# Performance work log

Measured on AMD Instinct MI355X. Metric: run time of the kernel, lower is better.

Reference implementation:

```python
import jax, jax.numpy as jnp
import numpy as np

B, T, D, H, F = 4, 2048, 512, 8, 2048
WINDOW = 128
HD = D // H
EPS = 1e-5


def layer_norm(x, g, b):
    mu = jnp.mean(x, axis=-1, keepdims=True)
    var = jnp.mean(jnp.square(x - mu), axis=-1, keepdims=True)
    return (x - mu) * jax.lax.rsqrt(var + EPS) * g + b


def setup_inputs() -> dict:
    key = jax.random.key(0)
    ks = jax.random.split(key, 5)
    s = 0.02
    return {
        "x": jax.random.normal(ks[0], (B, T, D), dtype=jnp.float32),
        "in_proj_w": jax.random.normal(ks[1], (3 * D, D), dtype=jnp.float32) * s,
        "in_proj_b": jnp.zeros((3 * D,), dtype=jnp.float32),
        "out_w": jax.random.normal(ks[2], (D, D), dtype=jnp.float32) * s,
        "out_b": jnp.zeros((D,), dtype=jnp.float32),
        "ln1_g": jnp.ones((D,), dtype=jnp.float32),
        "ln1_b": jnp.zeros((D,), dtype=jnp.float32),
        "ln2_g": jnp.ones((D,), dtype=jnp.float32),
        "ln2_b": jnp.zeros((D,), dtype=jnp.float32),
        "w1": jax.random.normal(ks[3], (F, D), dtype=jnp.float32) * s,
        "b1": jnp.zeros((F,), dtype=jnp.float32),
        "w2": jax.random.normal(ks[4], (D, F), dtype=jnp.float32) * s,
        "b2": jnp.zeros((D,), dtype=jnp.float32),
    }


def reference(x, in_proj_w, in_proj_b, out_w, out_b, ln1_g, ln1_b, ln2_g, ln2_b, w1, b1, w2, b2):
    # pre-norm sliding-window causal self-attention
    x2 = layer_norm(x, ln1_g, ln1_b)
    qkv = x2 @ in_proj_w.T + in_proj_b  # (B,T,3D)
    q, k, v = jnp.split(qkv, 3, axis=-1)
    q = q.reshape(B, T, H, HD)
    k = k.reshape(B, T, H, HD)
    v = v.reshape(B, T, H, HD)
    scale = 1.0 / np.sqrt(HD).astype(np.float32)
    scores = jnp.einsum("bthd,bshd->bhts", q, k) * scale  # dense (B,H,T,T)
    idx = jnp.arange(T)
    i = idx[:, None]
    j = idx[None, :]
    allowed = (j <= i) & (j >= i - WINDOW + 1)  # (T,T) bool, True = attend
    scores = jnp.where(allowed[None, None], scores, -jnp.inf)
    attn = jax.nn.softmax(scores, axis=-1)
    ctx = jnp.einsum("bhts,bshd->bthd", attn, v).reshape(B, T, D)
    attn_out = ctx @ out_w.T + out_b
    x = x + attn_out  # dropout is identity in eval
    # FFN block
    x3 = layer_norm(x, ln2_g, ln2_b)
    h = jax.nn.gelu(x3 @ w1.T + b1, approximate=False)
    x = x + h @ w2.T + b2
    return x
```

## Files before the change

kernel.cpp:

```cpp
#include <hip/hip_runtime.h>
#include <math.h>

constexpr int Bn = 4;
constexpr int Tn = 2048;
constexpr int Dn = 512;
constexpr int Hn = 8;
constexpr int HDn = 64;
constexpr int Fn = 2048;
constexpr int WIN = 128;
constexpr float EPS = 1e-5f;
constexpr int Mrows = Bn * Tn;
constexpr int QKVD = 3 * Dn;

using short8 = __attribute__((ext_vector_type(8))) short;
using f32x4  = __attribute__((ext_vector_type(4))) float;

__device__ __forceinline__ short f2bf(float f) {
    unsigned u = __float_as_uint(f);
    unsigned r = (u + 0x7FFFu + ((u >> 16) & 1u)) >> 16;
    return (short)r;
}

__device__ __forceinline__ float gelu_fast(float v) {
    float u = 1.5957691216f * v * (1.0f + 0.044715f * v * v);
    float t = 1.0f - 2.0f / (__expf(u) + 1.0f);
    return 0.5f * v * (1.0f + t);
}

__device__ __forceinline__ void async16(const short* g, short* l) {
    __builtin_amdgcn_global_load_lds(
        (const __attribute__((address_space(1))) void*)g,
        (__attribute__((address_space(3))) void*)l,
        16, 0, 0);
}

__global__ __launch_bounds__(256) void cvt_all(const float* __restrict__ s0,
                                               const float* __restrict__ s1,
                                               const float* __restrict__ s2,
                                               const float* __restrict__ s3,
                                               short* __restrict__ d0,
                                               short* __restrict__ d1,
                                               short* __restrict__ d2,
                                               short* __restrict__ d3)
{
    int i = blockIdx.x * 256 + threadIdx.x;
    const float* src; short* dst; int j;
    if (i < 196608)      { src = s0; dst = d0; j = i; }
    else if (i < 262144) { src = s1; dst = d1; j = i - 196608; }
    else if (i < 524288) { src = s2; dst = d2; j = i - 262144; }
    else                 { src = s3; dst = d3; j = i - 524288; }
    float4 v = ((const float4*)src)[j];
    short4 o;
    o.x = f2bf(v.x); o.y = f2bf(v.y); o.z = f2bf(v.z); o.w = f2bf(v.w);
    ((short4*)dst)[j] = o;
}

__global__ __launch_bounds__(64) void ln_kernel(const float* __restrict__ x,
                                                const float* __restrict__ g,
                                                const float* __restrict__ b,
                                                short* __restrict__ y)
{
    int row = blockIdx.x;
    int lane = threadIdx.x;
    const float4* xr = (const float4*)(x + (size_t)row * Dn);
    float4 v0 = xr[lane];
    float4 v1 = xr[lane + 64];
    float s = v0.x + v0.y + v0.z + v0.w + v1.x + v1.y + v1.z + v1.w;
#pragma unroll
    for (int off = 32; off >= 1; off >>= 1) s += __shfl_xor(s, off, 64);
    float mu = s * (1.0f / Dn);
    float d0x = v0.x - mu, d0y = v0.y - mu, d0z = v0.z - mu, d0w = v0.w - mu;
    float d1x = v1.x - mu, d1y = v1.y - mu, d1z = v1.z - mu, d1w = v1.w - mu;
    float q = d0x*d0x + d0y*d0y + d0z*d0z + d0w*d0w
            + d1x*d1x + d1y*d1y + d1z*d1z + d1w*d1w;
#pragma unroll
    for (int off = 32; off >= 1; off >>= 1) q += __shfl_xor(q, off, 64);
    float inv = rsqrtf(q * (1.0f / Dn) + EPS);
    const float4* gr = (const float4*)g;
    const float4* br = (const float4*)b;
    float4 g0 = gr[lane], g1 = gr[lane + 64];
    float4 b0 = br[lane], b1 = br[lane + 64];
    short4 a0, a1;
    a0.x = f2bf(d0x * inv * g0.x + b0.x);
    a0.y = f2bf(d0y * inv * g0.y + b0.y);
    a0.z = f2bf(d0z * inv * g0.z + b0.z);
    a0.w = f2bf(d0w * inv * g0.w + b0.w);
    a1.x = f2bf(d1x * inv * g1.x + b1.x);
    a1.y = f2bf(d1y * inv * g1.y + b1.y);
    a1.z = f2bf(d1z * inv * g1.z + b1.z);
    a1.w = f2bf(d1w * inv * g1.w + b1.w);
    short4* yr = (short4*)(y + (size_t)row * Dn);
    yr[lane] = a0;
    yr[lane + 64] = a1;
}

__global__ __launch_bounds__(256) void gemm_res(const short* __restrict__ A,
                                                const short* __restrict__ Bw,
                                                const float* __restrict__ bias,
                                                const float* __restrict__ resid,
                                                float* __restrict__ Cf,
                                                int M, int N, int K)
{
    constexpr int BK = 64;
    constexpr int NCH = 8;
    constexpr int BUF = 128 * BK;
    __shared__ short SMEM[4 * BUF];
    short* Asb = SMEM;
    short* Bsb = SMEM + 2 * BUF;

    int tid = threadIdx.x;
    int w = tid >> 6, lane = tid & 63;
    int wr = w >> 1, wc = w & 1;
    int nN = N >> 7;
    int bid = blockIdx.x;
    int xcd = bid & 7, sq = bid >> 3;
    int mi = xcd + 8 * (sq / nN);
    int ni = sq % nN;
    int m0 = mi * 128, n0 = ni * 128;
    int quad = lane >> 4, l16 = lane & 15;

    f32x4 zero = {0.f, 0.f, 0.f, 0.f};
    f32x4 acc[4][4];
#pragma unroll
    for (int i = 0; i < 4; ++i)
#pragma unroll
        for (int j = 0; j < 4; ++j) acc[i][j] = zero;

    int rl = lane >> 3;
    int ch = lane & 7;
    const short* Ag[4];
    const short* Bg[4];
    int ldsOff[4];
#pragma unroll
    for (int s = 0; s < 4; ++s) {
        int rowl = w * 32 + s * 8 + rl;
        int csw = (ch ^ (rowl & 7)) * 8;
        Ag[s] = A + (size_t)(m0 + rowl) * K + csw;
        Bg[s] = Bw + (size_t)(n0 + rowl) * K + csw;
        ldsOff[s] = (w * 32 + s * 8) * BK;
    }

    auto stage = [&](int kt, int pp) {
#pragma unroll
        for (int s = 0; s < 4; ++s) {
            async16(Ag[s] + kt, Asb + pp * BUF + ldsOff[s]);
            async16(Bg[s] + kt, Bsb + pp * BUF + ldsOff[s]);
        }
    };

    stage(0, 0);
    int p = 0;
    for (int kt = 0; kt < K; kt += BK) {
        __syncthreads();
        if (kt + BK < K) stage(kt + BK, p ^ 1);
        short8 aF[2][4], bF[2][4];
#pragma unroll
        for (int kk = 0; kk < 2; ++kk)
#pragma unroll
            for (int i = 0; i < 4; ++i) {
                int ra = wr * 64 + i * 16 + l16;
                int rb = wc * 64 + i * 16 + l16;
                int csA = ((kk * 4 + quad) ^ (ra & 7)) * 8;
                int csB = ((kk * 4 + quad) ^ (rb & 7)) * 8;
                aF[kk][i] = *(const short8*)(Asb + p * BUF + ra * BK + csA);
                bF[kk][i] = *(const short8*)(Bsb + p * BUF + rb * BK + csB);
            }
#pragma unroll
        for (int kk = 0; kk < 2; ++kk)
#pragma unroll
            for (int i = 0; i < 4; ++i)
#pragma unroll
                for (int j = 0; j < 4; ++j)
                    acc[i][j] = __builtin_amdgcn_mfma_f32_16x16x32_bf16(
                        aF[kk][i], bF[kk][j], acc[i][j], 0, 0, 0);
        p ^= 1;
    }

#pragma unroll
    for (int j = 0; j < 4; ++j) {
        int n = n0 + wc * 64 + j * 16 + l16;
        float bv = bias[n];
#pragma unroll
        for (int i = 0; i < 4; ++i) {
            int mbase = m0 + wr * 64 + i * 16 + quad * 4;
#pragma unroll
            for (int r = 0; r < 4; ++r) {
                size_t idx = (size_t)(mbase + r) * N + n;
                Cf[idx] = acc[i][j][r] + bv + resid[idx];
            }
        }
    }
}

template <int MODE>
__global__ __launch_bounds__(256, 2) void gemm_wide(const short* __restrict__ A,
                                                    const short* __restrict__ Bw,
                                                    const float* __restrict__ bias,
                                                    void* __restrict__ Cout,
                                                    short* __restrict__ q_out,
                                                    short* __restrict__ k_out,
                                                    short* __restrict__ v_out,
                                                    int M, int N, int K)
{
    constexpr int BK = 32;
    constexpr int ABUF = 128 * BK;
    constexpr int BBUF = 256 * BK;
    __shared__ short SMEM[2 * (ABUF + BBUF)];
    short* Asb = SMEM;
    short* Bsb = SMEM + 2 * ABUF;

    int tid = threadIdx.x;
    int w = tid >> 6, lane = tid & 63;
    int wr = w >> 1, wc = w & 1;
    int nT = N >> 8;
    int bid = blockIdx.x;
    int xcd = bid & 7, sq = bid >> 3;
    int mi = xcd + 8 * (sq / nT);
    int ni = sq % nT;
    int m0 = mi * 128, n0 = ni * 256;
    int quad = lane >> 4, l16 = lane & 15;

    f32x4 zero = {0.f, 0.f, 0.f, 0.f};
    f32x4 acc[4][8];
#pragma unroll
    for (int i = 0; i < 4; ++i)
#pragma unroll
        for (int j = 0; j < 8; ++j) acc[i][j] = zero;

    int rl = lane >> 2;
    int ch = lane & 3;
    const short* Ag[2];
    const short* Bg[4];
    int aOff[2], bOff[4];
#pragma unroll
    for (int s = 0; s < 2; ++s) {
        int rowl = w * 32 + s * 16 + rl;
        int csw = (ch ^ ((rowl >> 1) & 3)) * 8;
        Ag[s] = A + (size_t)(m0 + rowl) * K + csw;
        aOff[s] = (w * 32 + s * 16) * BK;
    }
#pragma unroll
    for (int s = 0; s < 4; ++s) {
        int rowl = w * 64 + s * 16 + rl;
        int csw = (ch ^ ((rowl >> 1) & 3)) * 8;
        Bg[s] = Bw + (size_t)(n0 + rowl) * K + csw;
        bOff[s] = (w * 64 + s * 16) * BK;
    }

    auto stage = [&](int kt, int pp) {
#pragma unroll
        for (int s = 0; s < 2; ++s)
            async16(Ag[s] + kt, Asb + pp * ABUF + aOff[s]);
#pragma unroll
        for (int s = 0; s < 4; ++s)
            async16(Bg[s] + kt, Bsb + pp * BBUF + bOff[s]);
    };

    int aoff[4], boff[8];
#pragma unroll
    for (int i = 0; i < 4; ++i) {
        int ra = wr * 64 + i * 16 + l16;
        aoff[i] = ra * BK + (quad ^ ((ra >> 1) & 3)) * 8;
    }
#pragma unroll
    for (int j = 0; j < 8; ++j) {
        int rb = wc * 128 + j * 16 + l16;
        boff[j] = rb * BK + (quad ^ ((rb >> 1) & 3)) * 8;
    }

    stage(0, 0);
    int p = 0;
    for (int kt = 0; kt < K; kt += BK) {
        __syncthreads();
        if (kt + BK < K) stage(kt + BK, p ^ 1);
        short8 aF[4], bF[8];
#pragma unroll
        for (int i = 0; i < 4; ++i)
            aF[i] = *(const short8*)(Asb + p * ABUF + aoff[i]);
#pragma unroll
        for (int j = 0; j < 8; ++j)
            bF[j] = *(const short8*)(Bsb + p * BBUF + boff[j]);
#pragma unroll
        for (int i = 0; i < 4; ++i)
#pragma unroll
            for (int j = 0; j < 8; ++j)
                acc[i][j] = __builtin_amdgcn_mfma_f32_16x16x32_bf16(
                    aF[i], bF[j], acc[i][j], 0, 0, 0);
        p ^= 1;
    }

    __syncthreads();
    short* rp = SMEM + w * 6144;
    float bv[8];
#pragma unroll
    for (int j = 0; j < 8; ++j) bv[j] = bias[n0 + wc * 128 + j * 16 + l16];

    if constexpr (MODE == 2) {
        short* Cb = (short*)Cout;
#pragma unroll
        for (int ph = 0; ph < 2; ++ph) {
#pragma unroll
            for (int i = 2 * ph; i < 2 * ph + 2; ++i) {
                int ml = (i - 2 * ph) * 16 + quad * 4;
#pragma unroll
                for (int j = 0; j < 8; ++j)
#pragma unroll
                    for (int r = 0; r < 4; ++r)
                        rp[(ml + r) * 136 + j * 16 + l16] =
                            f2bf(gelu_fast(acc[i][j][r] + bv[j]));
            }
#pragma unroll
            for (int it = 0; it < 8; ++it) {
                int row = it * 4 + (lane >> 4);
                int off = (lane & 15) * 8;
                *(short8*)(Cb + (size_t)(m0 + wr * 64 + 32 * ph + row) * N
                              + n0 + wc * 128 + off) =
                    *(const short8*)(rp + row * 136 + off);
            }
        }
        return;
    }

    if constexpr (MODE == 3) {
        int b = m0 >> 11;
        int ncol0 = n0 + wc * 128;
        int sec = ncol0 >> 9;
        int h0 = (ncol0 & 511) >> 6;
        int t0 = (m0 & 2047) + wr * 64;
        if (sec == 2) {
#pragma unroll
            for (int ph = 0; ph < 2; ++ph) {
#pragma unroll
                for (int j = 4 * ph; j < 4 * ph + 4; ++j) {
                    int d = (j - 4 * ph) * 16 + l16;
#pragma unroll
                    for (int i = 0; i < 4; ++i)
#pragma unroll
                        for (int r = 0; r < 4; ++r)
                            rp[d * 68 + i * 16 + quad * 4 + r] =
                                f2bf(acc[i][j][r] + bv[j]);
                }
                int bh = b * 8 + h0 + ph;
#pragma unroll
                for (int it = 0; it < 8; ++it) {
                    int drow = it * 8 + (lane >> 3);
                    int off = (lane & 7) * 8;
                    *(short8*)(v_out + ((size_t)bh * 64 + drow) * 2048 + t0 + off) =
                        *(const short8*)(rp + drow * 68 + off);
                }
            }
        } else {
            short* dst = (sec == 0 ? q_out : k_out);
#pragma unroll
            for (int ph = 0; ph < 2; ++ph) {
#pragma unroll
                for (int i = 2 * ph; i < 2 * ph + 2; ++i) {
                    int tl = (i - 2 * ph) * 16 + quad * 4;
#pragma unroll
                    for (int j = 0; j < 8; ++j)
#pragma unroll
                        for (int r = 0; r < 4; ++r)
                            rp[(tl + r) * 136 + j * 16 + l16] =
                                f2bf(acc[i][j][r] + bv[j]);
                }
#pragma unroll
                for (int it = 0; it < 8; ++it) {
                    int trow = it * 4 + (lane >> 4);
                    int hh = (lane & 15) >> 3;
                    int off = (lane & 7) * 8;
                    int bh = b * 8 + h0 + hh;
                    *(short8*)(dst + ((size_t)bh * 2048 + t0 + 32 * ph + trow) * 64 + off) =
                        *(const short8*)(rp + trow * 136 + hh * 64 + off);
                }
            }
        }
        return;
    }
}

constexpr int QS = 72;
constexpr int VS = 200;

__global__ __launch_bounds__(256) void attn_mfma(const short* __restrict__ Qg,
                                                 const short* __restrict__ Kg,
                                                 const short* __restrict__ Vtg,
                                                 short* __restrict__ ctx)
{
    __shared__ short Qs[64 * QS];
    __shared__ short Ks[192 * QS];
    __shared__ short Vt[64 * VS];
    int tid = threadIdx.x;
    int w = tid >> 6, lane = tid & 63, quad = lane >> 4, l16 = lane & 15;
    int blk = blockIdx.x;
    int q0 = (blk & 31) << 6;
    int bh = blk >> 5;
    int kbase = q0 - 128;

    {
        const short* src = Qg + ((size_t)bh * 2048 + q0) * 64;
        for (int c = tid; c < 512; c += 256) {
            int row = c >> 3, off = (c & 7) * 8;
            *(short8*)(Qs + row * QS + off) = *(const short8*)(src + row * 64 + off);
        }
    }
    {
        const short* base = Kg + (size_t)bh * 2048 * 64;
        for (int c = tid; c < 1536; c += 256) {
            int row = c >> 3, off = (c & 7) * 8;
            int srow = kbase + row; srow = srow < 0 ? 0 : srow;
            *(short8*)(Ks + row * QS + off) = *(const short8*)(base + (size_t)srow * 64 + off);
        }
    }
    {
        const short* base = Vtg + (size_t)bh * 64 * 2048;
        for (int c = tid; c < 1536; c += 256) {
            int row = c / 24, cc = c - row * 24;
            int off = cc * 8;
            int scol = kbase + off; scol = scol < 0 ? 0 : scol;
            *(short8*)(Vt + row * VS + off) = *(const short8*)(base + (size_t)row * 2048 + scol);
        }
    }
    __syncthreads();

    short8 aF0 = *(const short8*)(Qs + (w * 16 + l16) * QS + quad * 8);
    short8 aF1 = *(const short8*)(Qs + (w * 16 + l16) * QS + 32 + quad * 8);
    f32x4 S[12];
    f32x4 zero = {0.f, 0.f, 0.f, 0.f};
#pragma unroll
    for (int t = 0; t < 12; ++t) S[t] = zero;
#pragma unroll
    for (int t = 0; t < 12; ++t) {
        short8 b0 = *(const short8*)(Ks + (t * 16 + l16) * QS + quad * 8);
        short8 b1 = *(const short8*)(Ks + (t * 16 + l16) * QS + 32 + quad * 8);
        S[t] = __builtin_amdgcn_mfma_f32_16x16x32_bf16(aF0, b0, S[t], 0, 0, 0);
        S[t] = __builtin_amdgcn_mfma_f32_16x16x32_bf16(aF1, b1, S[t], 0, 0, 0);
    }

    int i0 = w * 16 + quad * 4;
    float mrow[4] = {-INFINITY, -INFINITY, -INFINITY, -INFINITY};
#pragma unroll
    for (int t = 0; t < 12; ++t) {
        int jl = t * 16 + l16;
        int kg = kbase + jl;
#pragma unroll
        for (int r = 0; r < 4; ++r) {
            int dj = jl - (i0 + r);
            bool ok = (dj >= 1) && (dj <= 128) && (kg >= 0);
            float s = ok ? S[t][r] * 0.125f : -INFINITY;
            S[t][r] = s;
            mrow[r] = fmaxf(mrow[r], s);
        }
    }
#pragma unroll
    for (int off = 8; off >= 1; off >>= 1)
#pragma unroll
        for (int r = 0; r < 4; ++r)
            mrow[r] = fmaxf(mrow[r], __shfl_xor(mrow[r], off, 64));
    float sum[4] = {0.f, 0.f, 0.f, 0.f};
#pragma unroll
    for (int t = 0; t < 12; ++t)
#pragma unroll
        for (int r = 0; r < 4; ++r) {
            float p = __expf(S[t][r] - mrow[r]);
            S[t][r] = p;
            sum[r] += p;
        }
#pragma unroll
    for (int off = 8; off >= 1; off >>= 1)
#pragma unroll
        for (int r = 0; r < 4; ++r)
            sum[r] += __shfl_xor(sum[r], off, 64);
    float inv[4];
#pragma unroll
    for (int r = 0; r < 4; ++r) inv[r] = 1.0f / sum[r];

    __syncthreads();
    short* Ps = Ks;
#pragma unroll
    for (int t = 0; t < 12; ++t)
#pragma unroll
        for (int r = 0; r < 4; ++r)
            Ps[(w * 16 + quad * 4 + r) * VS + t * 16 + l16] = f2bf(S[t][r]);

    f32x4 O[4];
#pragma unroll
    for (int tN = 0; tN < 4; ++tN) O[tN] = zero;
#pragma unroll
    for (int s = 0; s < 6; ++s) {
        short8 aP = *(const short8*)(Ps + (w * 16 + l16) * VS + s * 32 + quad * 8);
#pragma unroll
        for (int tN = 0; tN < 4; ++tN) {
            short8 bV = *(const short8*)(Vt + (tN * 16 + l16) * VS + s * 32 + quad * 8);
            O[tN] = __builtin_amdgcn_mfma_f32_16x16x32_bf16(aP, bV, O[tN], 0, 0, 0);
        }
    }

    int b = bh >> 3, h = bh & 7;
#pragma unroll
    for (int tN = 0; tN < 4; ++tN)
#pragma unroll
        for (int r = 0; r < 4; ++r) {
            int trow = q0 + w * 16 + quad * 4 + r;
            ctx[((size_t)(b * 2048 + trow)) * 512 + h * 64 + tN * 16 + l16] =
                f2bf(O[tN][r] * inv[r]);
        }
}

extern "C" void kernel_launch(void* const* d_in, const int* in_sizes, int n_in,
                              void* d_out, int out_size, void* d_ws, size_t ws_size,
                              hipStream_t stream)
{
    const float* x         = (const float*)d_in[0];
    const float* in_proj_w = (const float*)d_in[1];
    const float* in_proj_b = (const float*)d_in[2];
    const float* out_w     = (const float*)d_in[3];
    const float* out_b     = (const float*)d_in[4];
    const float* ln1_g     = (const float*)d_in[5];
    const float* ln1_b     = (const float*)d_in[6];
    const float* ln2_g     = (const float*)d_in[7];
    const float* ln2_b     = (const float*)d_in[8];
    const float* w1        = (const float*)d_in[9];
    const float* b1        = (const float*)d_in[10];
    const float* w2        = (const float*)d_in[11];
    const float* b2        = (const float*)d_in[12];
    float* out = (float*)d_out;

    char* ws = (char*)d_ws;
    short* attnQ = (short*)ws;
    short* attnK = (short*)(ws + (size_t)8 * 1024 * 1024);
    short* attnV = (short*)(ws + (size_t)16 * 1024 * 1024);
    short* hbuf  = (short*)ws;
    short* regB  = (short*)(ws + (size_t)32 * 1024 * 1024);
    short* wq  = (short*)(ws + (size_t)40 * 1024 * 1024);
    short* wo  = wq + (size_t)QKVD * Dn;
    short* w1b = wo + (size_t)Dn * Dn;
    short* w2b = w1b + (size_t)Fn * Dn;

    cvt_all<<<3072, 256, 0, stream>>>(in_proj_w, out_w, w1, w2, wq, wo, w1b, w2b);

    ln_kernel<<<Mrows, 64, 0, stream>>>(x, ln1_g, ln1_b, regB);
    gemm_wide<3><<<(Mrows / 128) * (QKVD / 256), 256, 0, stream>>>(
        regB, wq, in_proj_b, nullptr, attnQ, attnK, attnV, Mrows, QKVD, Dn);
    attn_mfma<<<Bn * Hn * (Tn / 64), 256, 0, stream>>>(attnQ, attnK, attnV, regB);
    gemm_res<<<(Mrows / 128) * (Dn / 128), 256, 0, stream>>>(
        regB, wo, out_b, x, out, Mrows, Dn, Dn);
    ln_kernel<<<Mrows, 64, 0, stream>>>(out, ln2_g, ln2_b, regB);
    gemm_wide<2><<<(Mrows / 128) * (Fn / 256), 256, 0, stream>>>(
        regB, w1b, b1, hbuf, nullptr, nullptr, nullptr, Mrows, Fn, Dn);
    gemm_res<<<(Mrows / 128) * (Dn / 128), 256, 0, stream>>>(
        hbuf, w2b, b2, out, out, Mrows, Dn, Fn);
}
```

Before: 215.9 us.

## Deepen gemm_res pipeline to 4-stage ring with BK=32 and vmcnt waits

Rewrites the residual GEMM main loop to use a four-slot LDS ring of BK=32 tiles with prefetch distance two. Each step uses explicit s_waitcnt vmcnt counts and a raw s_barrier in place of __syncthreads. The swizzle is reworked for 64-byte rows, and per-lane LDS read offsets are hoisted out of the loop. The goal is to overlap global loads with MFMA work and cut full barrier drains. The cost is twice as many loop iterations and barriers, and raw s_barrier with a distance-two prefetch into a four-slot ring depends on careful ordering to avoid LDS races.

Result: no change. 215.7 us (-0.1%).

```diff
diff --git a/kernel.cpp b/kernel.cpp
--- a/kernel.cpp
+++ b/kernel.cpp
@@ -101,13 +101,9 @@
                                                 float* __restrict__ Cf,
                                                 int M, int N, int K)
 {
-    constexpr int BK = 64;
-    constexpr int NCH = 8;
+    constexpr int BK = 32;
     constexpr int BUF = 128 * BK;
-    __shared__ short SMEM[4 * BUF];
-    short* Asb = SMEM;
-    short* Bsb = SMEM + 2 * BUF;
-
+    __shared__ short SMEM[8 * BUF];
     int tid = threadIdx.x;
     int w = tid >> 6, lane = tid & 63;
     int wr = w >> 1, wc = w & 1;
@@ -126,54 +122,68 @@
 #pragma unroll
         for (int j = 0; j < 4; ++j) acc[i][j] = zero;
 
-    int rl = lane >> 3;
-    int ch = lane & 7;
-    const short* Ag[4];
-    const short* Bg[4];
-    int ldsOff[4];
-#pragma unroll
-    for (int s = 0; s < 4; ++s) {
-        int rowl = w * 32 + s * 8 + rl;
-        int csw = (ch ^ (rowl & 7)) * 8;
+    int rl = lane >> 2;
+    int ch = lane & 3;
+    const short* Ag[2];
+    const short* Bg[2];
+    int ldsOff[2];
+#pragma unroll
+    for (int s = 0; s < 2; ++s) {
+        int rowl = w * 32 + s * 16 + rl;
+        int csw = (ch ^ ((rowl >> 1) & 3)) * 8;
         Ag[s] = A + (size_t)(m0 + rowl) * K + csw;
         Bg[s] = Bw + (size_t)(n0 + rowl) * K + csw;
-        ldsOff[s] = (w * 32 + s * 8) * BK;
-    }
-
-    auto stage = [&](int kt, int pp) {
-#pragma unroll
-        for (int s = 0; s < 4; ++s) {
-            async16(Ag[s] + kt, Asb + pp * BUF + ldsOff[s]);
-            async16(Bg[s] + kt, Bsb + pp * BUF + ldsOff[s]);
+        ldsOff[s] = (w * 32 + s * 16) * BK;
+    }
+
+    auto stage = [&](int kt, int qb) {
+        short* Ab = SMEM + qb * (2 * BUF);
+        short* Bb = Ab + BUF;
+#pragma unroll
+        for (int s = 0; s < 2; ++s) {
+            async16(Ag[s] + kt, Ab + ldsOff[s]);
+            async16(Bg[s] + kt, Bb + ldsOff[s]);
         }
     };
 
+    int aoff[4], boff[4];
+#pragma unroll
+    for (int i = 0; i < 4; ++i) {
+        int ra = wr * 64 + i * 16 + l16;
+        int rb = wc * 64 + i * 16 + l16;
+        aoff[i] = ra * BK + (quad ^ ((ra >> 1) & 3)) * 8;
+        boff[i] = rb * BK + (quad ^ ((rb >> 1) & 3)) * 8;
+    }
+
     stage(0, 0);
-    int p = 0;
-    for (int kt = 0; kt < K; kt += BK) {
-        __syncthreads();
-        if (kt + BK < K) stage(kt + BK, p ^ 1);
-        short8 aF[2][4], bF[2][4];
-#pragma unroll
-        for (int kk = 0; kk < 2; ++kk)
-#pragma unroll
-            for (int i = 0; i < 4; ++i) {
-                int ra = wr * 64 + i * 16 + l16;
-                int rb = wc * 64 + i * 16 + l16;
-                int csA = ((kk * 4 + quad) ^ (ra & 7)) * 8;
-                int csB = ((kk * 4 + quad) ^ (rb & 7)) * 8;
-                aF[kk][i] = *(const short8*)(Asb + p * BUF + ra * BK + csA);
-                bF[kk][i] = *(const short8*)(Bsb + p * BUF + rb * BK + csB);
-            }
-#pragma unroll
-        for (int kk = 0; kk < 2; ++kk)
-#pragma unroll
-            for (int i = 0; i < 4; ++i)
-#pragma unroll
-                for (int j = 0; j < 4; ++j)
-                    acc[i][j] = __builtin_amdgcn_mfma_f32_16x16x32_bf16(
-                        aF[kk][i], bF[kk][j], acc[i][j], 0, 0, 0);
-        p ^= 1;
+    stage(BK, 1);
+    int q = 0;
+    int t = 0;
+    for (int kt = 0; kt < K; kt += BK, ++t) {
+        if (kt + 2 * BK < K) {
+            stage(kt + 2 * BK, (t + 2) & 3);
+            asm volatile("s_waitcnt vmcnt(8)" ::: "memory");
+        } else if (kt + BK < K) {
+            asm volatile("s_waitcnt vmcnt(4)" ::: "memory");
+        } else {
+            asm volatile("s_waitcnt vmcnt(0)" ::: "memory");
+        }
+        asm volatile("s_barrier" ::: "memory");
+        const short* Ab = SMEM + q * (2 * BUF);
+        const short* Bb = Ab + BUF;
+        short8 aF[4], bF[4];
+#pragma unroll
+        for (int i = 0; i < 4; ++i) {
+            aF[i] = *(const short8*)(Ab + aoff[i]);
+            bF[i] = *(const short8*)(Bb + boff[i]);
+        }
+#pragma unroll
+        for (int i = 0; i < 4; ++i)
+#pragma unroll
+            for (int j = 0; j < 4; ++j)
+                acc[i][j] = __builtin_amdgcn_mfma_f32_16x16x32_bf16(
+                    aF[i], bF[j], acc[i][j], 0, 0, 0);
+        q = (q + 1) & 3;
     }
 
 #pragma unroll
```

## Halve gemm_res M tile, fuse weight conversion with LN1, batch LN rows

Applied to the files above, without the earlier changes.

The residual GEMM tile drops from 128x128 to 64x128, which doubles the block count for the N=512 output GEMMs so they fill the CUs with more than one wave and hide latency better. Weight bf16 conversion and the first layer norm are merged into one launch. Layer norm now processes four rows per 256-thread block instead of one row per 64-thread block. The smaller tile reloads the B operand more often, lowering data reuse per block.

Result: no change. 216.2 us (+0.1%).

```diff
diff --git a/kernel.cpp b/kernel.cpp
--- a/kernel.cpp
+++ b/kernel.cpp
@@ -34,35 +34,12 @@
         16, 0, 0);
 }
 
-__global__ __launch_bounds__(256) void cvt_all(const float* __restrict__ s0,
-                                               const float* __restrict__ s1,
-                                               const float* __restrict__ s2,
-                                               const float* __restrict__ s3,
-                                               short* __restrict__ d0,
-                                               short* __restrict__ d1,
-                                               short* __restrict__ d2,
-                                               short* __restrict__ d3)
-{
-    int i = blockIdx.x * 256 + threadIdx.x;
-    const float* src; short* dst; int j;
-    if (i < 196608)      { src = s0; dst = d0; j = i; }
-    else if (i < 262144) { src = s1; dst = d1; j = i - 196608; }
-    else if (i < 524288) { src = s2; dst = d2; j = i - 262144; }
-    else                 { src = s3; dst = d3; j = i - 524288; }
-    float4 v = ((const float4*)src)[j];
-    short4 o;
-    o.x = f2bf(v.x); o.y = f2bf(v.y); o.z = f2bf(v.z); o.w = f2bf(v.w);
-    ((short4*)dst)[j] = o;
-}
-
-__global__ __launch_bounds__(64) void ln_kernel(const float* __restrict__ x,
-                                                const float* __restrict__ g,
-                                                const float* __restrict__ b,
-                                                short* __restrict__ y)
-{
-    int row = blockIdx.x;
-    int lane = threadIdx.x;
-    const float4* xr = (const float4*)(x + (size_t)row * Dn);
+__device__ __forceinline__ void ln_row(const float* __restrict__ xrow,
+                                       const float* __restrict__ g,
+                                       const float* __restrict__ b,
+                                       short* __restrict__ yrow, int lane)
+{
+    const float4* xr = (const float4*)xrow;
     float4 v0 = xr[lane];
     float4 v1 = xr[lane + 64];
     float s = v0.x + v0.y + v0.z + v0.w + v1.x + v1.y + v1.z + v1.w;
@@ -89,9 +66,51 @@
     a1.y = f2bf(d1y * inv * g1.y + b1.y);
     a1.z = f2bf(d1z * inv * g1.z + b1.z);
     a1.w = f2bf(d1w * inv * g1.w + b1.w);
-    short4* yr = (short4*)(y + (size_t)row * Dn);
+    short4* yr = (short4*)yrow;
     yr[lane] = a0;
     yr[lane + 64] = a1;
+}
+
+__global__ __launch_bounds__(256) void prep_kernel(const float* __restrict__ s0,
+                                                   const float* __restrict__ s1,
+                                                   const float* __restrict__ s2,
+                                                   const float* __restrict__ s3,
+                                                   short* __restrict__ d0,
+                                                   short* __restrict__ d1,
+                                                   short* __restrict__ d2,
+                                                   short* __restrict__ d3,
+                                                   const float* __restrict__ x,
+                                                   const float* __restrict__ ln1_g,
+                                                   const float* __restrict__ ln1_b,
+                                                   short* __restrict__ x2)
+{
+    int bid = blockIdx.x;
+    if (bid < 3072) {
+        int i = bid * 256 + threadIdx.x;
+        const float* src; short* dst; int j;
+        if (i < 196608)      { src = s0; dst = d0; j = i; }
+        else if (i < 262144) { src = s1; dst = d1; j = i - 196608; }
+        else if (i < 524288) { src = s2; dst = d2; j = i - 262144; }
+        else                 { src = s3; dst = d3; j = i - 524288; }
+        float4 v = ((const float4*)src)[j];
+        short4 o;
+        o.x = f2bf(v.x); o.y = f2bf(v.y); o.z = f2bf(v.z); o.w = f2bf(v.w);
+        ((short4*)dst)[j] = o;
+    } else {
+        int row = (bid - 3072) * 4 + (threadIdx.x >> 6);
+        int lane = threadIdx.x & 63;
+        ln_row(x + (size_t)row * Dn, ln1_g, ln1_b, x2 + (size_t)row * Dn, lane);
+    }
+}
+
+__global__ __launch_bounds__(256) void ln_kernel(const float* __restrict__ x,
+                                                 const float* __restrict__ g,
+                                                 const float* __restrict__ b,
+                                                 short* __restrict__ y)
+{
+    int row = blockIdx.x * 4 + (threadIdx.x >> 6);
+    int lane = threadIdx.x & 63;
+    ln_row(x + (size_t)row * Dn, g, b, y + (size_t)row * Dn, lane);
 }
 
 __global__ __launch_bounds__(256) void gemm_res(const short* __restrict__ A,
@@ -102,11 +121,11 @@
                                                 int M, int N, int K)
 {
     constexpr int BK = 64;
-    constexpr int NCH = 8;
-    constexpr int BUF = 128 * BK;
-    __shared__ short SMEM[4 * BUF];
+    constexpr int ABUF = 64 * BK;
+    constexpr int BBUF = 128 * BK;
+    __shared__ short SMEM[2 * (ABUF + BBUF)];
     short* Asb = SMEM;
-    short* Bsb = SMEM + 2 * BUF;
+    short* Bsb = SMEM + 2 * ABUF;
 
     int tid = threadIdx.x;
     int w = tid >> 6, lane = tid & 63;
@@ -116,59 +135,82 @@
     int xcd = bid & 7, sq = bid >> 3;
     int mi = xcd + 8 * (sq / nN);
     int ni = sq % nN;
-    int m0 = mi * 128, n0 = ni * 128;
+    int m0 = mi * 64, n0 = ni * 128;
     int quad = lane >> 4, l16 = lane & 15;
 
     f32x4 zero = {0.f, 0.f, 0.f, 0.f};
-    f32x4 acc[4][4];
-#pragma unroll
-    for (int i = 0; i < 4; ++i)
+    f32x4 acc[2][4];
+#pragma unroll
+    for (int i = 0; i < 2; ++i)
 #pragma unroll
         for (int j = 0; j < 4; ++j) acc[i][j] = zero;
 
     int rl = lane >> 3;
     int ch = lane & 7;
-    const short* Ag[4];
+    const short* Ag[2];
     const short* Bg[4];
-    int ldsOff[4];
+    int aOff[2], bOff[4];
+#pragma unroll
+    for (int s = 0; s < 2; ++s) {
+        int rowl = w * 16 + s * 8 + rl;
+        int csw = (ch ^ (rowl & 7)) * 8;
+        Ag[s] = A + (size_t)(m0 + rowl) * K + csw;
+        aOff[s] = (w * 16 + s * 8) * BK;
+    }
 #pragma unroll
     for (int s = 0; s < 4; ++s) {
         int rowl = w * 32 + s * 8 + rl;
         int csw = (ch ^ (rowl & 7)) * 8;
-        Ag[s] = A + (size_t)(m0 + rowl) * K + csw;
         Bg[s] = Bw + (size_t)(n0 + rowl) * K + csw;
-        ldsOff[s] = (w * 32 + s * 8) * BK;
+        bOff[s] = (w * 32 + s * 8) * BK;
     }
 
     auto stage = [&](int kt, int pp) {
 #pragma unroll
-        for (int s = 0; s < 4; ++s) {
-            async16(Ag[s] + kt, Asb + pp * BUF + ldsOff[s]);
-            async16(Bg[s] + kt, Bsb + pp * BUF + ldsOff[s]);
-        }
+        for (int s = 0; s < 2; ++s)
+            async16(Ag[s] + kt, Asb + pp * ABUF + aOff[s]);
+#pragma unroll
+        for (int s = 0; s < 4; ++s)
+            async16(Bg[s] + kt, Bsb + pp * BBUF + bOff[s]);
     };
+
+    int aoff[2], boff[4];
+#pragma unroll
+    for (int i = 0; i < 2; ++i) {
+        int ra = wr * 32 + i * 16 + l16;
+        aoff[i] = ra * BK;
+    }
+#pragma unroll
+    for (int j = 0; j < 4; ++j) {
+        int rb = wc * 64 + j * 16 + l16;
+        boff[j] = rb * BK;
+    }
 
     stage(0, 0);
     int p = 0;
     for (int kt = 0; kt < K; kt += BK) {
         __syncthreads();
         if (kt + BK < K) stage(kt + BK, p ^ 1);
-        short8 aF[2][4], bF[2][4];
+        short8 aF[2][2], bF[2][4];
+#pragma unroll
+        for (int kk = 0; kk < 2; ++kk) {
+#pragma unroll
+            for (int i = 0; i < 2; ++i) {
+                int ra = wr * 32 + i * 16 + l16;
+                int cs = ((kk * 4 + quad) ^ (ra & 7)) * 8;
+                aF[kk][i] = *(const short8*)(Asb + p * ABUF + aoff[i] + cs);
+            }
+#pragma unroll
+            for (int j = 0; j < 4; ++j) {
+                int rb = wc * 64 + j * 16 + l16;
+                int cs = ((kk * 4 + quad) ^ (rb & 7)) * 8;
+                bF[kk][j] = *(const short8*)(Bsb + p * BBUF + boff[j] + cs);
+            }
+        }
 #pragma unroll
         for (int kk = 0; kk < 2; ++kk)
 #pragma unroll
-            for (int i = 0; i < 4; ++i) {
-                int ra = wr * 64 + i * 16 + l16;
-                int rb = wc * 64 + i * 16 + l16;
-                int csA = ((kk * 4 + quad) ^ (ra & 7)) * 8;
-                int csB = ((kk * 4 + quad) ^ (rb & 7)) * 8;
-                aF[kk][i] = *(const short8*)(Asb + p * BUF + ra * BK + csA);
-                bF[kk][i] = *(const short8*)(Bsb + p * BUF + rb * BK + csB);
-            }
-#pragma unroll
-        for (int kk = 0; kk < 2; ++kk)
-#pragma unroll
-            for (int i = 0; i < 4; ++i)
+            for (int i = 0; i < 2; ++i)
 #pragma unroll
                 for (int j = 0; j < 4; ++j)
                     acc[i][j] = __builtin_amdgcn_mfma_f32_16x16x32_bf16(
@@ -181,8 +223,8 @@
         int n = n0 + wc * 64 + j * 16 + l16;
         float bv = bias[n];
 #pragma unroll
-        for (int i = 0; i < 4; ++i) {
-            int mbase = m0 + wr * 64 + i * 16 + quad * 4;
+        for (int i = 0; i < 2; ++i) {
+            int mbase = m0 + wr * 32 + i * 16 + quad * 4;
 #pragma unroll
             for (int r = 0; r < 4; ++r) {
                 size_t idx = (size_t)(mbase + r) * N + n;
@@ -536,17 +578,16 @@
     short* w1b = wo + (size_t)Dn * Dn;
     short* w2b = w1b + (size_t)Fn * Dn;
 
-    cvt_all<<<3072, 256, 0, stream>>>(in_proj_w, out_w, w1, w2, wq, wo, w1b, w2b);
-
-    ln_kernel<<<Mrows, 64, 0, stream>>>(x, ln1_g, ln1_b, regB);
+    prep_kernel<<<5120, 256, 0, stream>>>(in_proj_w, out_w, w1, w2, wq, wo, w1b, w2b,
+                                          x, ln1_g, ln1_b, regB);
     gemm_wide<3><<<(Mrows / 128) * (QKVD / 256), 256, 0, stream>>>(
         regB, wq, in_proj_b, nullptr, attnQ, attnK, attnV, Mrows, QKVD, Dn);
     attn_mfma<<<Bn * Hn * (Tn / 64), 256, 0, stream>>>(attnQ, attnK, attnV, regB);
-    gemm_res<<<(Mrows / 128) * (Dn / 128), 256, 0, stream>>>(
+    gemm_res<<<(Mrows / 64) * (Dn / 128), 256, 0, stream>>>(
         regB, wo, out_b, x, out, Mrows, Dn, Dn);
-    ln_kernel<<<Mrows, 64, 0, stream>>>(out, ln2_g, ln2_b, regB);
+    ln_kernel<<<Mrows / 4, 256, 0, stream>>>(out, ln2_g, ln2_b, regB);
     gemm_wide<2><<<(Mrows / 128) * (Fn / 256), 256, 0, stream>>>(
         regB, w1b, b1, hbuf, nullptr, nullptr, nullptr, Mrows, Fn, Dn);
-    gemm_res<<<(Mrows / 128) * (Dn / 128), 256, 0, stream>>>(
+    gemm_res<<<(Mrows / 64) * (Dn / 128), 256, 0, stream>>>(
         hbuf, w2b, b2, out, out, Mrows, Dn, Fn);
 }
```
